# Optimization experiments

Measured on AMD Instinct MI355X. Metric: run time of the kernel, lower is better.

The kernel has to match this reference:

```python
import jax, jax.numpy as jnp
import numpy as np

B, G, D, E = 16, 2048, 2048, 32          # batch, genes, drug fp dim, gene embed dim
NL, NM, H, GS = 16, 4, 6, 64             # n leaves, n mids, term hidden, genes per leaf
GAMMA, NDRUG, EPS = 0.5, 1024, 1e-5

def _bn3(x):  # BatchNorm1d on [B, C, L], training stats, affine at init (gamma=1, beta=0)
    m = x.mean(axis=(0, 2), keepdims=True)
    v = x.var(axis=(0, 2), keepdims=True)
    return (x - m) / jnp.sqrt(v + EPS)

def _bn2(x):  # BatchNorm1d on [B, C]
    m = x.mean(axis=0, keepdims=True)
    v = x.var(axis=0, keepdims=True)
    return (x - m) / jnp.sqrt(v + EPS)

def _term(ci, W1, b1, Wc, bc, Wd, bd):
    # ci: [B, E, in] child input; returns ([B,H,E] 3d out, [B,H] 2d out)
    h = jnp.einsum('bei,hi->bhe', ci, W1) + b1[None, :, None]      # linear -> permute
    h = _bn3(h)
    c = jnp.einsum('bhe,kh->bke', h, Wc) + bc[None, :, None]       # context layer
    out3d = _bn3(c)                                                # [B,H,E]
    mean = out3d.mean(axis=1)                                      # [B,E]
    out2d = _bn2(jnp.tanh(mean @ Wd.T + bd))                       # dimension layer
    return out3d, out2d

def setup_inputs():
    key = jax.random.key(0)
    ks = iter(jax.random.split(key, 64))
    def rn(shape):
        return jax.random.normal(next(ks), shape, dtype=jnp.float32) * 0.05
    x = jax.random.normal(next(ks), (B, G + D + 1), dtype=jnp.float32)
    idx = jax.random.randint(next(ks), (B,), 0, NDRUG)
    x = x.at[:, -1].set(idx.astype(jnp.float32))
    table = jax.random.randint(next(ks), (NDRUG, G), 0, G, dtype=jnp.int32)
    inp = dict(x=x, table=table,
        W_rbf=rn((E, G)), b_rbf=rn((E,)), emb=rn((G, E)),
        W_dg=rn((NL, GS, G)), b_dg=rn((NL, GS)),
        Wl1=rn((NL, H, GS)), bl1=rn((NL, H)), Wlc=rn((NL, H, H)), blc=rn((NL, H)),
        Wld=rn((NL, H, E)), bld=rn((NL, H)),
        Wm1=rn((NM, H, 4 * H)), bm1=rn((NM, H)), Wmc=rn((NM, H, H)), bmc=rn((NM, H)),
        Wmd=rn((NM, H, E)), bmd=rn((NM, H)),
        Wr1=rn((H, 4 * H)), br1=rn((H,)), Wrc=rn((H, H)), brc=rn((H,)),
        Wrd=rn((H, E)), brd=rn((H,)),
        Wd1=rn((100, D)), bd1=rn((100,)), Wd2=rn((50, 100)), bd2=rn((50,)),
        Wd3=rn((H, 50)), bd3=rn((H,)),
        Wf=rn((6, 2 * H)), bf=rn((6,)), Wfa=rn((1, 6)), bfa=rn((1,)),
        Wfo=rn((1, 1)), bfo=rn((1,)))
    return inp

def reference(x, W_rbf, b_rbf, emb, W_dg, b_dg,
              Wl1, bl1, Wlc, blc, Wld, bld,
              Wm1, bm1, Wmc, bmc, Wmd, bmd,
              Wr1, br1, Wrc, brc, Wrd, brd,
              Wd1, bd1, Wd2, bd2, Wd3, bd3,
              Wf, bf, Wfa, bfa, Wfo, bfo, table):
    g = x[:, :G]
    drug = x[:, G:G + D]
    idx = x[:, G + D].astype(jnp.int32)
    # RBF kernel: [B, G, G]
    vect = jnp.exp(-GAMMA * jnp.square(g[:, :, None] - g[:, None, :]))
    gv = jnp.einsum('bij,ej->bie', vect, W_rbf) + b_rbf            # [B,G,E]
    lv = emb[table[idx]]                                            # [B,G,E]
    gf = (gv + lv).transpose(0, 2, 1)                               # [B,E,G]
    # per-leaf direct gene layers
    gene_out = jnp.einsum('beg,lkg->lbek', gf, W_dg) + b_dg[:, None, None, :]  # [NL,B,E,GS]
    leaf3d, _ = jax.vmap(_term)(gene_out, Wl1, bl1, Wlc, blc, Wld, bld)        # [NL,B,H,E]
    # mid terms: concat 4 leaf children along feature dim
    a = leaf3d.transpose(0, 1, 3, 2).reshape(NM, 4, B, E, H)
    a = jnp.moveaxis(a, 1, 3).reshape(NM, B, E, 4 * H)
    mid3d, _ = jax.vmap(_term)(a, Wm1, bm1, Wmc, bmc, Wmd, bmd)                # [NM,B,H,E]
    r = jnp.moveaxis(mid3d.transpose(0, 1, 3, 2), 0, 2).reshape(B, E, 4 * H)
    _, root2d = _term(r, Wr1, br1, Wrc, brc, Wrd, brd)                          # [B,H]
    # drug MLP
    d = drug
    for Wl, bl in ((Wd1, bd1), (Wd2, bd2), (Wd3, bd3)):
        d = _bn2(jnp.tanh(d @ Wl.T + bl))
    fin = jnp.concatenate([root2d, d], axis=1)                                  # [B,2H]
    out = _bn2(jnp.tanh(fin @ Wf.T + bf))
    aux = jnp.tanh(out @ Wfa.T + bfa)
    return aux @ Wfo.T + bfo                                                    # [B,1]
```

## Files before the change

### kernel.cpp

```cpp
#include <hip/hip_runtime.h>
#include <hip/hip_bf16.h>

#define Bb 16
#define Gg 2048
#define Dd 2048
#define XS 4097
#define EPSf 1e-5f
#define CEXP (-0.72134752044448170368f)

typedef unsigned int u32;
typedef __attribute__((ext_vector_type(8))) short bf16x8;
typedef __attribute__((ext_vector_type(4))) float f32x4;

union U16 { uint4 u; bf16x8 v; };

__device__ inline float fast_exp2(float x) {
#if __has_builtin(__builtin_amdgcn_exp2f)
  return __builtin_amdgcn_exp2f(x);
#else
  return exp2f(x);
#endif
}

__device__ inline u32 pk2(float a, float b) {
  return __builtin_amdgcn_perm(__float_as_uint(b), __float_as_uint(a), 0x07060302u);
}
__device__ inline float bftrunc(float a) {
  return __uint_as_float(__float_as_uint(a) & 0xFFFF0000u);
}

__device__ inline void split8(const float* f, U16& hi, U16& lo) {
  u32 h[4], l[4];
  #pragma unroll
  for (int p = 0; p < 4; ++p) {
    float a = f[2 * p], b = f[2 * p + 1];
    h[p] = pk2(a, b);
    l[p] = pk2(a - bftrunc(a), b - bftrunc(b));
  }
  hi.u = make_uint4(h[0], h[1], h[2], h[3]);
  lo.u = make_uint4(l[0], l[1], l[2], l[3]);
}

__device__ inline float wred(float v) {
  #pragma unroll
  for (int o = 32; o > 0; o >>= 1) v += __shfl_xor(v, o, 64);
  return v;
}

__global__ __launch_bounds__(256) void k_split(const float* __restrict__ Wrbf,
                                               const float* __restrict__ Wdg,
                                               u32* __restrict__ Rhi, u32* __restrict__ Rlo,
                                               u32* __restrict__ Dhi, u32* __restrict__ Dlo) {
  int c = blockIdx.x * 256 + threadIdx.x;
  const float* src;
  u32 *dhi, *dlo;
  if (c < 8192) {
    int h = c >> 12, ks = (c >> 6) & 63, l = c & 63;
    src = Wrbf + (h * 16 + (l & 15)) * Gg + ks * 32 + (l >> 4) * 8;
    dhi = Rhi + (size_t)c * 4; dlo = Rlo + (size_t)c * 4;
  } else {
    int cc = c - 8192;
    int nf = cc >> 12, ks = (cc >> 6) & 63, l = cc & 63;
    src = Wdg + (size_t)(nf * 16 + (l & 15)) * Gg + ks * 32 + (l >> 4) * 8;
    dhi = Dhi + (size_t)cc * 4; dlo = Dlo + (size_t)cc * 4;
  }
  float4 f0 = *(const float4*)src;
  float4 f1 = *(const float4*)(src + 4);
  float f[8] = {f0.x, f0.y, f0.z, f0.w, f1.x, f1.y, f1.z, f1.w};
  U16 hi, lo;
  split8(f, hi, lo);
  *(uint4*)dhi = hi.u;
  *(uint4*)dlo = lo.u;
}

__global__ __launch_bounds__(1024) void k_rbf2(const float* __restrict__ x,
                                               const u32* __restrict__ Whi,
                                               const u32* __restrict__ Wlo,
                                               const int* __restrict__ table,
                                               const float* __restrict__ emb,
                                               const float* __restrict__ brbf,
                                               u32* __restrict__ Ahi,
                                               u32* __restrict__ Alo) {
  __shared__ float g_s[2048];
  __shared__ float red[16][64][8];
  const int tid = threadIdx.x;
  const int lane = tid & 63, wid = tid >> 6;
  const int isub = wid >> 2, jcw = wid & 3;
  const int i0 = blockIdx.x * 64, b = blockIdx.y;
  const int i0w = i0 + isub * 16;
  g_s[tid] = x[(size_t)b * XS + tid];
  g_s[tid + 1024] = x[(size_t)b * XS + 1024 + tid];
  const float gi = x[(size_t)b * XS + i0w + (lane & 15)];
  f32x4 acc0 = {0.f, 0.f, 0.f, 0.f};
  f32x4 acc1 = {0.f, 0.f, 0.f, 0.f};
  const int jb = (lane >> 4) * 8;
  __syncthreads();

  #pragma unroll
  for (int ksl = 0; ksl < 16; ++ksl) {
    const int ks = jcw * 16 + ksl;
    const float* gp = &g_s[ks * 32 + jb];
    float4 gja = *(const float4*)gp;
    float4 gjb = *(const float4*)(gp + 4);
    float gv[8] = {gja.x, gja.y, gja.z, gja.w, gjb.x, gjb.y, gjb.z, gjb.w};
    float kv[8];
    #pragma unroll
    for (int q = 0; q < 8; ++q) {
      float d = gi - gv[q];
      kv[q] = fast_exp2(d * d * CEXP);
    }
    U16 ah, al;
    split8(kv, ah, al);
    U16 w0h, w1h, w0l, w1l;
    const size_t wo = (size_t)ks * 256 + lane * 4;
    w0h.u = *(const uint4*)(Whi + wo);
    w1h.u = *(const uint4*)(Whi + 16384 + wo);
    w0l.u = *(const uint4*)(Wlo + wo);
    w1l.u = *(const uint4*)(Wlo + 16384 + wo);
    acc0 = __builtin_amdgcn_mfma_f32_16x16x32_bf16(ah.v, w0h.v, acc0, 0, 0, 0);
    acc0 = __builtin_amdgcn_mfma_f32_16x16x32_bf16(al.v, w0h.v, acc0, 0, 0, 0);
    acc0 = __builtin_amdgcn_mfma_f32_16x16x32_bf16(ah.v, w0l.v, acc0, 0, 0, 0);
    acc1 = __builtin_amdgcn_mfma_f32_16x16x32_bf16(ah.v, w1h.v, acc1, 0, 0, 0);
    acc1 = __builtin_amdgcn_mfma_f32_16x16x32_bf16(al.v, w1h.v, acc1, 0, 0, 0);
    acc1 = __builtin_amdgcn_mfma_f32_16x16x32_bf16(ah.v, w1l.v, acc1, 0, 0, 0);
  }
  #pragma unroll
  for (int k = 0; k < 4; ++k) { red[wid][lane][k] = acc0[k]; red[wid][lane][4 + k] = acc1[k]; }
  __syncthreads();
  if (jcw == 0) {
    float f[8];
    #pragma unroll
    for (int k = 0; k < 8; ++k)
      f[k] = red[isub * 4][lane][k] + red[isub * 4 + 1][lane][k] +
             red[isub * 4 + 2][lane][k] + red[isub * 4 + 3][lane][k];
    const int idx = (int)x[(size_t)b * XS + Gg + Dd];
    const int eloc = lane & 15, quad = lane >> 4;
    const int ib = i0w + quad * 4;
    int4 tt = *(const int4*)&table[(size_t)idx * Gg + ib];
    const int ks = i0w >> 5;
    const int lp = (2 * ((i0w >> 4) & 1) + (quad >> 1)) * 16 + eloc;
    const int hs = quad & 1;
    #pragma unroll
    for (int hb = 0; hb < 2; ++hb) {
      const int e = hb * 16 + eloc;
      const float bias = brbf[e];
      float v0 = f[hb * 4 + 0] + bias + emb[tt.x * 32 + e];
      float v1 = f[hb * 4 + 1] + bias + emb[tt.y * 32 + e];
      float v2 = f[hb * 4 + 2] + bias + emb[tt.z * 32 + e];
      float v3 = f[hb * 4 + 3] + bias + emb[tt.w * 32 + e];
      size_t off = (((size_t)(b * 2 + hb) * 64 + ks) * 64 + lp) * 4 + hs * 2;
      Ahi[off]     = pk2(v0, v1);
      Ahi[off + 1] = pk2(v2, v3);
      Alo[off]     = pk2(v0 - bftrunc(v0), v1 - bftrunc(v1));
      Alo[off + 1] = pk2(v2 - bftrunc(v2), v3 - bftrunc(v3));
    }
  }
}

__global__ __launch_bounds__(512) void k_mm(const u32* __restrict__ Ahi,
                                            const u32* __restrict__ Alo,
                                            const u32* __restrict__ Bhi,
                                            const u32* __restrict__ Blo,
                                            float* __restrict__ part) {
  __shared__ u32 s_mm[6144];
  const int tid = threadIdx.x;
  const int lane = tid & 63, wid = tid >> 6;
  const int id = blockIdx.x;
  const int pl = id & 7, by = (id >> 3) & 7, ph = id >> 6;
  const int p = ph * 8 + pl;
  const int bx = p >> 2, kc = p & 3;
  const int wm = wid >> 2, wn = wid & 3;
  f32x4 acc[2][2];
  #pragma unroll
  for (int mf = 0; mf < 2; ++mf)
    #pragma unroll
    for (int nf = 0; nf < 2; ++nf) acc[mf][nf] = (f32x4){0.f, 0.f, 0.f, 0.f};

  uint4 pf[3];
  #pragma unroll
  for (int q = 0; q < 3; ++q) {
    int seg = wid * 3 + q;
    const u32* src;
    if (seg < 8) {
      int hl = seg >> 2, mf = seg & 3;
      src = (hl ? Alo : Ahi) + (((size_t)(by * 4 + mf) * 64 + kc * 16) * 64 + lane) * 4;
    } else {
      int t = seg - 8, hl = t >> 3, nf = t & 7;
      src = (hl ? Blo : Bhi) + (((size_t)(bx * 8 + nf) * 64 + kc * 16) * 64 + lane) * 4;
    }
    pf[q] = *(const uint4*)src;
  }
  for (int stage = 0; stage < 16; ++stage) {
    __syncthreads();
    #pragma unroll
    for (int q = 0; q < 3; ++q)
      *(uint4*)&s_mm[(wid * 3 + q) * 256 + lane * 4] = pf[q];
    if (stage < 15) {
      const int ks = kc * 16 + stage + 1;
      #pragma unroll
      for (int q = 0; q < 3; ++q) {
        int seg = wid * 3 + q;
        const u32* src;
        if (seg < 8) {
          int hl = seg >> 2, mf = seg & 3;
          src = (hl ? Alo : Ahi) + (((size_t)(by * 4 + mf) * 64 + ks) * 64 + lane) * 4;
        } else {
          int t = seg - 8, hl = t >> 3, nf = t & 7;
          src = (hl ? Blo : Bhi) + (((size_t)(bx * 8 + nf) * 64 + ks) * 64 + lane) * 4;
        }
        pf[q] = *(const uint4*)src;
      }
    }
    __syncthreads();
    U16 ah[2], al[2], bh[2], bl[2];
    #pragma unroll
    for (int mf = 0; mf < 2; ++mf) {
      ah[mf].u = *(const uint4*)&s_mm[(0 + wm * 2 + mf) * 256 + lane * 4];
      al[mf].u = *(const uint4*)&s_mm[(4 + wm * 2 + mf) * 256 + lane * 4];
    }
    #pragma unroll
    for (int nf = 0; nf < 2; ++nf) {
      bh[nf].u = *(const uint4*)&s_mm[(8 + wn * 2 + nf) * 256 + lane * 4];
      bl[nf].u = *(const uint4*)&s_mm[(16 + wn * 2 + nf) * 256 + lane * 4];
    }
    #pragma unroll
    for (int mf = 0; mf < 2; ++mf) {
      #pragma unroll
      for (int nf = 0; nf < 2; ++nf) {
        acc[mf][nf] = __builtin_amdgcn_mfma_f32_16x16x32_bf16(ah[mf].v, bh[nf].v, acc[mf][nf], 0, 0, 0);
        acc[mf][nf] = __builtin_amdgcn_mfma_f32_16x16x32_bf16(al[mf].v, bh[nf].v, acc[mf][nf], 0, 0, 0);
        acc[mf][nf] = __builtin_amdgcn_mfma_f32_16x16x32_bf16(ah[mf].v, bl[nf].v, acc[mf][nf], 0, 0, 0);
      }
    }
  }
  const int quad = lane >> 4, nl = lane & 15;
  #pragma unroll
  for (int mf = 0; mf < 2; ++mf) {
    #pragma unroll
    for (int nf = 0; nf < 2; ++nf) {
      int n  = bx * 128 + wn * 32 + nf * 16 + nl;
      int m0 = by * 64 + wm * 32 + mf * 16 + quad * 4;
      float4 st = make_float4(acc[mf][nf][0], acc[mf][nf][1], acc[mf][nf][2], acc[mf][nf][3]);
      *(float4*)&part[(size_t)kc * 524288 + (size_t)n * 512 + m0] = st;
    }
  }
}

__device__ inline void bn512(float* v, int wv, int lane,
                             float (*r1)[6], float (*r2)[6]) {
  float s[6], q[6];
  #pragma unroll
  for (int c = 0; c < 6; ++c) {
    float a = v[c];
    s[c] = wred(a);
    q[c] = wred(a * a);
  }
  __syncthreads();
  if (lane == 0) {
    #pragma unroll
    for (int c = 0; c < 6; ++c) { r1[wv][c] = s[c]; r2[wv][c] = q[c]; }
  }
  __syncthreads();
  #pragma unroll
  for (int c = 0; c < 6; ++c) {
    float S = 0.f, Q = 0.f;
    #pragma unroll
    for (int w = 0; w < 8; ++w) { S += r1[w][c]; Q += r2[w][c]; }
    float m  = S * (1.0f / 512.0f);
    float va = Q * (1.0f / 512.0f) - m * m;
    v[c] = (v[c] - m) * rsqrtf(va + EPSf);
  }
}

__global__ __launch_bounds__(512) void k_leaf(const float* __restrict__ part,
                                              const float* __restrict__ bdg,
                                              const float* __restrict__ W1,
                                              const float* __restrict__ b1,
                                              const float* __restrict__ Wc,
                                              const float* __restrict__ bc,
                                              float* __restrict__ outp) {
  const int l = blockIdx.x, tid = threadIdx.x;
  const int wv = tid >> 6, lane = tid & 63;
  __shared__ float r1[8][6], r2[8][6];
  float cv[64];
  #pragma unroll
  for (int i = 0; i < 64; ++i) {
    int n = l * 64 + i;
    const float* pp = part + (size_t)n * 512 + tid;
    cv[i] = pp[0] + pp[524288] + pp[2 * 524288] + pp[3 * 524288] + bdg[n];
  }
  const float* w1 = W1 + l * 6 * 64;
  float h[6];
  #pragma unroll
  for (int hh = 0; hh < 6; ++hh) {
    float s = b1[l * 6 + hh];
    #pragma unroll
    for (int i = 0; i < 64; ++i) s = fmaf(cv[i], w1[hh * 64 + i], s);
    h[hh] = s;
  }
  bn512(h, wv, lane, r1, r2);
  float c[6];
  #pragma unroll
  for (int k = 0; k < 6; ++k) {
    float s = bc[l * 6 + k];
    #pragma unroll
    for (int hh = 0; hh < 6; ++hh) s = fmaf(h[hh], Wc[l * 36 + k * 6 + hh], s);
    c[k] = s;
  }
  bn512(c, wv, lane, r1, r2);
  float* o = outp + (((size_t)(l >> 2) * 512 + tid) * 24 + (l & 3) * 6);
  #pragma unroll
  for (int k = 0; k < 6; ++k) o[k] = c[k];
}

__global__ __launch_bounds__(512) void k_mid(const float* __restrict__ gin,
                                             const float* __restrict__ W1,
                                             const float* __restrict__ b1,
                                             const float* __restrict__ Wc,
                                             const float* __restrict__ bc,
                                             float* __restrict__ outp) {
  const int l = blockIdx.x, tid = threadIdx.x;
  const int wv = tid >> 6, lane = tid & 63;
  __shared__ float r1[8][6], r2[8][6];
  const float* ci = gin + ((size_t)l * 512 + tid) * 24;
  float cv[24];
  #pragma unroll
  for (int q = 0; q < 6; ++q) *(float4*)&cv[q * 4] = ((const float4*)ci)[q];
  const float* w1 = W1 + l * 6 * 24;
  float h[6];
  #pragma unroll
  for (int hh = 0; hh < 6; ++hh) {
    float s = b1[l * 6 + hh];
    #pragma unroll
    for (int i = 0; i < 24; ++i) s = fmaf(cv[i], w1[hh * 24 + i], s);
    h[hh] = s;
  }
  bn512(h, wv, lane, r1, r2);
  float c[6];
  #pragma unroll
  for (int k = 0; k < 6; ++k) {
    float s = bc[l * 6 + k];
    #pragma unroll
    for (int hh = 0; hh < 6; ++hh) s = fmaf(h[hh], Wc[l * 36 + k * 6 + hh], s);
    c[k] = s;
  }
  bn512(c, wv, lane, r1, r2);
  float* o = outp + ((size_t)tid * 24 + l * 6);
  #pragma unroll
  for (int k = 0; k < 6; ++k) o[k] = c[k];
}

__global__ __launch_bounds__(1024) void k_drug1(const float* __restrict__ x,
                                                const float* __restrict__ Wd1,
                                                const float* __restrict__ bd1,
                                                float* __restrict__ d1) {
  const int c = blockIdx.x;
  const int tid = threadIdx.x;
  const int b = tid >> 6, lane = tid & 63;
  const float* xb = x + (size_t)b * XS + Gg;
  const float* w = Wd1 + (size_t)c * 2048;
  float s = 0.f;
  #pragma unroll
  for (int q = 0; q < 8; ++q) {
    int k = q * 256 + lane * 4;
    float4 xv = *(const float4*)(xb + k);
    float4 wv = *(const float4*)(w + k);
    s = fmaf(xv.x, wv.x, s);
    s = fmaf(xv.y, wv.y, s);
    s = fmaf(xv.z, wv.z, s);
    s = fmaf(xv.w, wv.w, s);
  }
  s = wred(s);
  __shared__ float y[16];
  if (lane == 0) y[b] = tanhf(s + bd1[c]);
  __syncthreads();
  if (tid < 16) {
    float S = 0.f, Q = 0.f;
    #pragma unroll
    for (int bb = 0; bb < 16; ++bb) { float v = y[bb]; S += v; Q += v * v; }
    float m = S * (1.0f / 16.0f), va = Q * (1.0f / 16.0f) - m * m;
    d1[tid * 100 + c] = (y[tid] - m) * rsqrtf(va + EPSf);
  }
}

__global__ __launch_bounds__(512) void k_rootfinal(const float* __restrict__ rootin,
                                                   const float* __restrict__ d1,
                                                   const float* __restrict__ Wr1,
                                                   const float* __restrict__ br1,
                                                   const float* __restrict__ Wrc,
                                                   const float* __restrict__ brc,
                                                   const float* __restrict__ Wrd,
                                                   const float* __restrict__ brd,
                                                   const float* __restrict__ Wd2,
                                                   const float* __restrict__ bd2,
                                                   const float* __restrict__ Wd3,
                                                   const float* __restrict__ bd3,
                                                   const float* __restrict__ Wf,
                                                   const float* __restrict__ bf,
                                                   const float* __restrict__ Wfa,
                                                   const float* __restrict__ bfa,
                                                   const float* __restrict__ Wfo,
                                                   const float* __restrict__ bfo,
                                                   float* __restrict__ out) {
  const int tid = threadIdx.x;
  const int wv = tid >> 6, lane = tid & 63;
  __shared__ float r1[8][6], r2[8][6];
  __shared__ float w2s[50 * 101];
  __shared__ float d1s[1600];
  __shared__ float r2ds[96];
  for (int u = tid; u < 5000; u += 512) w2s[(u / 100) * 101 + (u % 100)] = Wd2[u];
  for (int u = tid; u < 1600; u += 512) d1s[u] = d1[u];

  const float* ci = rootin + (size_t)tid * 24;
  float cv[24];
  #pragma unroll
  for (int q = 0; q < 6; ++q) *(float4*)&cv[q * 4] = ((const float4*)ci)[q];
  float h[6];
  #pragma unroll
  for (int hh = 0; hh < 6; ++hh) {
    float s = br1[hh];
    #pragma unroll
    for (int i = 0; i < 24; ++i) s = fmaf(cv[i], Wr1[hh * 24 + i], s);
    h[hh] = s;
  }
  bn512(h, wv, lane, r1, r2);
  float c[6];
  #pragma unroll
  for (int k = 0; k < 6; ++k) {
    float s = brc[k];
    #pragma unroll
    for (int hh = 0; hh < 6; ++hh) s = fmaf(h[hh], Wrc[k * 6 + hh], s);
    c[k] = s;
  }
  bn512(c, wv, lane, r1, r2);
  float mv = (c[0] + c[1] + c[2] + c[3] + c[4] + c[5]) * (1.0f / 6.0f);
  __shared__ float shm[512];
  shm[tid] = mv;
  __syncthreads();
  __shared__ float st[96];
  if (tid < 96) {
    int b = tid / 6, hh = tid % 6;
    float s = brd[hh];
    #pragma unroll
    for (int e = 0; e < 32; ++e) s = fmaf(shm[b * 32 + e], Wrd[hh * 32 + e], s);
    st[tid] = tanhf(s);
  }
  __syncthreads();
  if (tid < 6) {
    float S = 0.f, Q = 0.f;
    for (int b = 0; b < 16; ++b) { float v = st[b * 6 + tid]; S += v; Q += v * v; }
    float m = S * (1.0f / 16.0f), va = Q * (1.0f / 16.0f) - m * m;
    float iv = rsqrtf(va + EPSf);
    for (int b = 0; b < 16; ++b) r2ds[b * 6 + tid] = (st[b * 6 + tid] - m) * iv;
  }
  __syncthreads();

  __shared__ float s2[800], mu2[50], iv2[50];
  for (int u = tid; u < 800; u += 512) {
    int b = u / 50, cc = u % 50;
    float s = bd2[cc];
    #pragma unroll
    for (int k = 0; k < 100; ++k) s = fmaf(d1s[b * 100 + k], w2s[cc * 101 + k], s);
    s2[u] = tanhf(s);
  }
  __syncthreads();
  if (tid < 50) {
    float S = 0.f, Q = 0.f;
    #pragma unroll
    for (int b = 0; b < 16; ++b) { float v = s2[b * 50 + tid]; S += v; Q += v * v; }
    float m = S * (1.0f / 16.0f), va = Q * (1.0f / 16.0f) - m * m;
    mu2[tid] = m; iv2[tid] = rsqrtf(va + EPSf);
  }
  __syncthreads();
  __shared__ float s3[96], mu3[6], iv3[6];
  if (tid < 96) {
    int b = tid / 6, cc = tid % 6;
    float s = bd3[cc];
    #pragma unroll
    for (int k = 0; k < 50; ++k)
      s = fmaf((s2[b * 50 + k] - mu2[k]) * iv2[k], Wd3[cc * 50 + k], s);
    s3[tid] = tanhf(s);
  }
  __syncthreads();
  if (tid < 6) {
    float S = 0.f, Q = 0.f;
    #pragma unroll
    for (int b = 0; b < 16; ++b) { float v = s3[b * 6 + tid]; S += v; Q += v * v; }
    float m = S * (1.0f / 16.0f), va = Q * (1.0f / 16.0f) - m * m;
    mu3[tid] = m; iv3[tid] = rsqrtf(va + EPSf);
  }
  __syncthreads();
  __shared__ float sf[96], muf[6], ivf[6];
  if (tid < 96) {
    int b = tid / 6, cc = tid % 6;
    float s = bf[cc];
    #pragma unroll
    for (int q = 0; q < 6; ++q) s = fmaf(r2ds[b * 6 + q], Wf[cc * 12 + q], s);
    #pragma unroll
    for (int q = 0; q < 6; ++q)
      s = fmaf((s3[b * 6 + q] - mu3[q]) * iv3[q], Wf[cc * 12 + 6 + q], s);
    sf[tid] = tanhf(s);
  }
  __syncthreads();
  if (tid < 6) {
    float S = 0.f, Q = 0.f;
    #pragma unroll
    for (int b = 0; b < 16; ++b) { float v = sf[b * 6 + tid]; S += v; Q += v * v; }
    float m = S * (1.0f / 16.0f), va = Q * (1.0f / 16.0f) - m * m;
    muf[tid] = m; ivf[tid] = rsqrtf(va + EPSf);
  }
  __syncthreads();
  if (tid < 16) {
    float s = bfa[0];
    #pragma unroll
    for (int q = 0; q < 6; ++q)
      s = fmaf((sf[tid * 6 + q] - muf[q]) * ivf[q], Wfa[q], s);
    float a = tanhf(s);
    out[tid] = a * Wfo[0] + bfo[0];
  }
}

extern "C" void kernel_launch(void* const* d_in, const int* in_sizes, int n_in,
                              void* d_out, int out_size, void* d_ws, size_t ws_size,
                              hipStream_t stream) {
  const float* x     = (const float*)d_in[0];
  const int*   table = (const int*)d_in[1];
  const float* Wrbf  = (const float*)d_in[2];
  const float* brbf  = (const float*)d_in[3];
  const float* emb   = (const float*)d_in[4];
  const float* Wdg   = (const float*)d_in[5];
  const float* bdg   = (const float*)d_in[6];
  const float* Wl1   = (const float*)d_in[7];
  const float* bl1   = (const float*)d_in[8];
  const float* Wlc   = (const float*)d_in[9];
  const float* blc   = (const float*)d_in[10];
  const float* Wm1   = (const float*)d_in[13];
  const float* bm1   = (const float*)d_in[14];
  const float* Wmc   = (const float*)d_in[15];
  const float* bmc   = (const float*)d_in[16];
  const float* Wr1   = (const float*)d_in[19];
  const float* br1   = (const float*)d_in[20];
  const float* Wrc   = (const float*)d_in[21];
  const float* brc   = (const float*)d_in[22];
  const float* Wrd   = (const float*)d_in[23];
  const float* brd   = (const float*)d_in[24];
  const float* Wd1   = (const float*)d_in[25];
  const float* bd1   = (const float*)d_in[26];
  const float* Wd2   = (const float*)d_in[27];
  const float* bd2   = (const float*)d_in[28];
  const float* Wd3   = (const float*)d_in[29];
  const float* bd3   = (const float*)d_in[30];
  const float* Wf    = (const float*)d_in[31];
  const float* bf    = (const float*)d_in[32];
  const float* Wfa   = (const float*)d_in[33];
  const float* bfa   = (const float*)d_in[34];
  const float* Wfo   = (const float*)d_in[35];
  const float* bfo   = (const float*)d_in[36];
  float* out = (float*)d_out;

  u32* Rhi = (u32*)d_ws;
  u32* Rlo = Rhi + 32768;
  u32* Dhi = Rlo + 32768;
  u32* Dlo = Dhi + 1048576;
  u32* Ahi = Dlo + 1048576;
  u32* Alo = Ahi + 524288;
  float* partB = (float*)(Alo + 524288);
  float* midin = partB + 4 * 524288;
  float* rootin= midin + 49152;
  float* d1    = rootin + 12288;

  hipLaunchKernelGGL(k_drug1,     dim3(100),    dim3(1024), 0, stream, x, Wd1, bd1, d1);
  hipLaunchKernelGGL(k_split,     dim3(1056),   dim3(256),  0, stream, Wrbf, Wdg, Rhi, Rlo, Dhi, Dlo);
  hipLaunchKernelGGL(k_rbf2,      dim3(32, 16), dim3(1024), 0, stream, x, Rhi, Rlo, table, emb, brbf, Ahi, Alo);
  hipLaunchKernelGGL(k_mm,        dim3(256),    dim3(512),  0, stream, Ahi, Alo, Dhi, Dlo, partB);
  hipLaunchKernelGGL(k_leaf,      dim3(16),     dim3(512),  0, stream, partB, bdg, Wl1, bl1, Wlc, blc, midin);
  hipLaunchKernelGGL(k_mid,       dim3(4),      dim3(512),  0, stream, midin, Wm1, bm1, Wmc, bmc, rootin);
  hipLaunchKernelGGL(k_rootfinal, dim3(1),      dim3(512),  0, stream, rootin, d1,
                     Wr1, br1, Wrc, brc, Wrd, brd, Wd2, bd2, Wd3, bd3,
                     Wf, bf, Wfa, bfa, Wfo, bfo, out);
}
```

Measured before the change: 115.6 us.

## Merge drug and split kernels, stage rbf weights in LDS, split leaf reduction

```diff
diff --git a/kernel.cpp b/kernel.cpp
--- a/kernel.cpp
+++ b/kernel.cpp
@@ -47,33 +47,67 @@
   return v;
 }
 
-__global__ __launch_bounds__(256) void k_split(const float* __restrict__ Wrbf,
-                                               const float* __restrict__ Wdg,
-                                               u32* __restrict__ Rhi, u32* __restrict__ Rlo,
-                                               u32* __restrict__ Dhi, u32* __restrict__ Dlo) {
-  int c = blockIdx.x * 256 + threadIdx.x;
-  const float* src;
-  u32 *dhi, *dlo;
-  if (c < 8192) {
-    int h = c >> 12, ks = (c >> 6) & 63, l = c & 63;
-    src = Wrbf + (h * 16 + (l & 15)) * Gg + ks * 32 + (l >> 4) * 8;
-    dhi = Rhi + (size_t)c * 4; dlo = Rlo + (size_t)c * 4;
+__global__ __launch_bounds__(1024) void k_pre(const float* __restrict__ x,
+                                              const float* __restrict__ Wd1,
+                                              const float* __restrict__ bd1,
+                                              float* __restrict__ d1,
+                                              const float* __restrict__ Wrbf,
+                                              const float* __restrict__ Wdg,
+                                              u32* __restrict__ Rhi, u32* __restrict__ Rlo,
+                                              u32* __restrict__ Dhi, u32* __restrict__ Dlo) {
+  const int tid = threadIdx.x;
+  if (blockIdx.x < 100) {
+    const int c = blockIdx.x;
+    const int b = tid >> 6, lane = tid & 63;
+    const float* xb = x + (size_t)b * XS + Gg;
+    const float* w = Wd1 + (size_t)c * 2048;
+    float s = 0.f;
+    #pragma unroll
+    for (int q = 0; q < 8; ++q) {
+      int k = q * 256 + lane * 4;
+      float4 xv = *(const float4*)(xb + k);
+      float4 wv = *(const float4*)(w + k);
+      s = fmaf(xv.x, wv.x, s);
+      s = fmaf(xv.y, wv.y, s);
+      s = fmaf(xv.z, wv.z, s);
+      s = fmaf(xv.w, wv.w, s);
+    }
+    s = wred(s);
+    __shared__ float y[16];
+    if (lane == 0) y[b] = tanhf(s + bd1[c]);
+    __syncthreads();
+    if (tid < 16) {
+      float S = 0.f, Q = 0.f;
+      #pragma unroll
+      for (int bb = 0; bb < 16; ++bb) { float v = y[bb]; S += v; Q += v * v; }
+      float m = S * (1.0f / 16.0f), va = Q * (1.0f / 16.0f) - m * m;
+      d1[tid * 100 + c] = (y[tid] - m) * rsqrtf(va + EPSf);
+    }
   } else {
-    int cc = c - 8192;
-    int nf = cc >> 12, ks = (cc >> 6) & 63, l = cc & 63;
-    src = Wdg + (size_t)(nf * 16 + (l & 15)) * Gg + ks * 32 + (l >> 4) * 8;
-    dhi = Dhi + (size_t)cc * 4; dlo = Dlo + (size_t)cc * 4;
-  }
-  float4 f0 = *(const float4*)src;
-  float4 f1 = *(const float4*)(src + 4);
-  float f[8] = {f0.x, f0.y, f0.z, f0.w, f1.x, f1.y, f1.z, f1.w};
-  U16 hi, lo;
-  split8(f, hi, lo);
-  *(uint4*)dhi = hi.u;
-  *(uint4*)dlo = lo.u;
-}
-
-__global__ __launch_bounds__(1024) void k_rbf2(const float* __restrict__ x,
+    int c = (blockIdx.x - 100) * 1024 + tid;
+    const float* src;
+    u32 *dhi, *dlo;
+    if (c < 8192) {
+      int h = c >> 12, ks = (c >> 6) & 63, l = c & 63;
+      src = Wrbf + (h * 16 + (l & 15)) * Gg + ks * 32 + (l >> 4) * 8;
+      dhi = Rhi + (size_t)c * 4; dlo = Rlo + (size_t)c * 4;
+    } else {
+      int cc = c - 8192;
+      int nf = cc >> 12, ks = (cc >> 6) & 63, l = cc & 63;
+      src = Wdg + (size_t)(nf * 16 + (l & 15)) * Gg + ks * 32 + (l >> 4) * 8;
+      dhi = Dhi + (size_t)cc * 4; dlo = Dlo + (size_t)cc * 4;
+    }
+    float4 f0 = *(const float4*)src;
+    float4 f1 = *(const float4*)(src + 4);
+    float f[8] = {f0.x, f0.y, f0.z, f0.w, f1.x, f1.y, f1.z, f1.w};
+    U16 hi, lo;
+    split8(f, hi, lo);
+    *(uint4*)dhi = hi.u;
+    *(uint4*)dlo = lo.u;
+  }
+}
+
+__global__ __launch_bounds__(1024) void k_rbf3(const float* __restrict__ x,
                                                const u32* __restrict__ Whi,
                                                const u32* __restrict__ Wlo,
                                                const int* __restrict__ table,
@@ -82,7 +116,8 @@
                                                u32* __restrict__ Ahi,
                                                u32* __restrict__ Alo) {
   __shared__ float g_s[2048];
-  __shared__ float red[16][64][8];
+  __shared__ u32 w_s[2][16][256];
+  float (*red)[64][8] = (float (*)[64][8]) & w_s[0][0][0];
   const int tid = threadIdx.x;
   const int lane = tid & 63, wid = tid >> 6;
   const int isub = wid >> 2, jcw = wid & 3;
@@ -94,10 +129,16 @@
   f32x4 acc0 = {0.f, 0.f, 0.f, 0.f};
   f32x4 acc1 = {0.f, 0.f, 0.f, 0.f};
   const int jb = (lane >> 4) * 8;
-  __syncthreads();
-
-  #pragma unroll
+
+  const int jcw_s = wid >> 2, arr2_s = wid & 3;
+  const u32* wsrc = ((arr2_s & 2) ? Wlo : Whi) + ((arr2_s & 1) ? 16384 : 0);
+  uint4 pf = *(const uint4*)(wsrc + ((size_t)(jcw_s * 16)) * 256 + lane * 4);
+
   for (int ksl = 0; ksl < 16; ++ksl) {
+    *(uint4*)&w_s[ksl & 1][wid][lane * 4] = pf;
+    if (ksl < 15)
+      pf = *(const uint4*)(wsrc + ((size_t)(jcw_s * 16 + ksl + 1)) * 256 + lane * 4);
+    __syncthreads();
     const int ks = jcw * 16 + ksl;
     const float* gp = &g_s[ks * 32 + jb];
     float4 gja = *(const float4*)gp;
@@ -112,11 +153,10 @@
     U16 ah, al;
     split8(kv, ah, al);
     U16 w0h, w1h, w0l, w1l;
-    const size_t wo = (size_t)ks * 256 + lane * 4;
-    w0h.u = *(const uint4*)(Whi + wo);
-    w1h.u = *(const uint4*)(Whi + 16384 + wo);
-    w0l.u = *(const uint4*)(Wlo + wo);
-    w1l.u = *(const uint4*)(Wlo + 16384 + wo);
+    w0h.u = *(const uint4*)&w_s[ksl & 1][jcw * 4 + 0][lane * 4];
+    w1h.u = *(const uint4*)&w_s[ksl & 1][jcw * 4 + 1][lane * 4];
+    w0l.u = *(const uint4*)&w_s[ksl & 1][jcw * 4 + 2][lane * 4];
+    w1l.u = *(const uint4*)&w_s[ksl & 1][jcw * 4 + 3][lane * 4];
     acc0 = __builtin_amdgcn_mfma_f32_16x16x32_bf16(ah.v, w0h.v, acc0, 0, 0, 0);
     acc0 = __builtin_amdgcn_mfma_f32_16x16x32_bf16(al.v, w0h.v, acc0, 0, 0, 0);
     acc0 = __builtin_amdgcn_mfma_f32_16x16x32_bf16(ah.v, w0l.v, acc0, 0, 0, 0);
@@ -124,6 +164,7 @@
     acc1 = __builtin_amdgcn_mfma_f32_16x16x32_bf16(al.v, w1h.v, acc1, 0, 0, 0);
     acc1 = __builtin_amdgcn_mfma_f32_16x16x32_bf16(ah.v, w1l.v, acc1, 0, 0, 0);
   }
+  __syncthreads();
   #pragma unroll
   for (int k = 0; k < 4; ++k) { red[wid][lane][k] = acc0[k]; red[wid][lane][4 + k] = acc1[k]; }
   __syncthreads();
@@ -272,31 +313,43 @@
   }
 }
 
-__global__ __launch_bounds__(512) void k_leaf(const float* __restrict__ part,
-                                              const float* __restrict__ bdg,
-                                              const float* __restrict__ W1,
-                                              const float* __restrict__ b1,
-                                              const float* __restrict__ Wc,
-                                              const float* __restrict__ bc,
-                                              float* __restrict__ outp) {
+__global__ __launch_bounds__(512) void k_leafA(const float* __restrict__ part,
+                                               const float* __restrict__ bdg,
+                                               const float* __restrict__ W1,
+                                               float* __restrict__ hpart) {
+  const int ic = blockIdx.x, l = blockIdx.y, tid = threadIdx.x;
+  const float* w1 = W1 + l * 384;
+  float hp[6] = {0.f, 0.f, 0.f, 0.f, 0.f, 0.f};
+  #pragma unroll
+  for (int r = 0; r < 8; ++r) {
+    int i = ic * 8 + r;
+    int n = l * 64 + i;
+    const float* pp = part + (size_t)n * 512 + tid;
+    float cv = pp[0] + pp[524288] + pp[2 * 524288] + pp[3 * 524288] + bdg[n];
+    #pragma unroll
+    for (int hh = 0; hh < 6; ++hh) hp[hh] = fmaf(cv, w1[hh * 64 + i], hp[hh]);
+  }
+  float* o = hpart + ((size_t)(l * 8 + ic) * 512 + tid) * 6;
+  #pragma unroll
+  for (int hh = 0; hh < 6; ++hh) o[hh] = hp[hh];
+}
+
+__global__ __launch_bounds__(512) void k_leafB(const float* __restrict__ hpart,
+                                               const float* __restrict__ b1,
+                                               const float* __restrict__ Wc,
+                                               const float* __restrict__ bc,
+                                               float* __restrict__ outp) {
   const int l = blockIdx.x, tid = threadIdx.x;
   const int wv = tid >> 6, lane = tid & 63;
   __shared__ float r1[8][6], r2[8][6];
-  float cv[64];
-  #pragma unroll
-  for (int i = 0; i < 64; ++i) {
-    int n = l * 64 + i;
-    const float* pp = part + (size_t)n * 512 + tid;
-    cv[i] = pp[0] + pp[524288] + pp[2 * 524288] + pp[3 * 524288] + bdg[n];
-  }
-  const float* w1 = W1 + l * 6 * 64;
   float h[6];
   #pragma unroll
-  for (int hh = 0; hh < 6; ++hh) {
-    float s = b1[l * 6 + hh];
-    #pragma unroll
-    for (int i = 0; i < 64; ++i) s = fmaf(cv[i], w1[hh * 64 + i], s);
-    h[hh] = s;
+  for (int hh = 0; hh < 6; ++hh) h[hh] = b1[l * 6 + hh];
+  #pragma unroll
+  for (int ic = 0; ic < 8; ++ic) {
+    const float* hp = hpart + ((size_t)(l * 8 + ic) * 512 + tid) * 6;
+    #pragma unroll
+    for (int hh = 0; hh < 6; ++hh) h[hh] += hp[hh];
   }
   bn512(h, wv, lane, r1, r2);
   float c[6];
@@ -348,39 +401,6 @@
   float* o = outp + ((size_t)tid * 24 + l * 6);
   #pragma unroll
   for (int k = 0; k < 6; ++k) o[k] = c[k];
-}
-
-__global__ __launch_bounds__(1024) void k_drug1(const float* __restrict__ x,
-                                                const float* __restrict__ Wd1,
-                                                const float* __restrict__ bd1,
-                                                float* __restrict__ d1) {
-  const int c = blockIdx.x;
-  const int tid = threadIdx.x;
-  const int b = tid >> 6, lane = tid & 63;
-  const float* xb = x + (size_t)b * XS + Gg;
-  const float* w = Wd1 + (size_t)c * 2048;
-  float s = 0.f;
-  #pragma unroll
-  for (int q = 0; q < 8; ++q) {
-    int k = q * 256 + lane * 4;
-    float4 xv = *(const float4*)(xb + k);
-    float4 wv = *(const float4*)(w + k);
-    s = fmaf(xv.x, wv.x, s);
-    s = fmaf(xv.y, wv.y, s);
-    s = fmaf(xv.z, wv.z, s);
-    s = fmaf(xv.w, wv.w, s);
-  }
-  s = wred(s);
-  __shared__ float y[16];
-  if (lane == 0) y[b] = tanhf(s + bd1[c]);
-  __syncthreads();
-  if (tid < 16) {
-    float S = 0.f, Q = 0.f;
-    #pragma unroll
-    for (int bb = 0; bb < 16; ++bb) { float v = y[bb]; S += v; Q += v * v; }
-    float m = S * (1.0f / 16.0f), va = Q * (1.0f / 16.0f) - m * m;
-    d1[tid * 100 + c] = (y[tid] - m) * rsqrtf(va + EPSf);
-  }
 }
 
 __global__ __launch_bounds__(512) void k_rootfinal(const float* __restrict__ rootin,
@@ -565,15 +585,18 @@
   u32* Ahi = Dlo + 1048576;
   u32* Alo = Ahi + 524288;
   float* partB = (float*)(Alo + 524288);
-  float* midin = partB + 4 * 524288;
+  float* hpart = partB + 4 * 524288;
+  float* midin = hpart + 393216;
   float* rootin= midin + 49152;
   float* d1    = rootin + 12288;
 
-  hipLaunchKernelGGL(k_drug1,     dim3(100),    dim3(1024), 0, stream, x, Wd1, bd1, d1);
-  hipLaunchKernelGGL(k_split,     dim3(1056),   dim3(256),  0, stream, Wrbf, Wdg, Rhi, Rlo, Dhi, Dlo);
-  hipLaunchKernelGGL(k_rbf2,      dim3(32, 16), dim3(1024), 0, stream, x, Rhi, Rlo, table, emb, brbf, Ahi, Alo);
+  hipLaunchKernelGGL(k_pre,       dim3(364),    dim3(1024), 0, stream,
+                     x, Wd1, bd1, d1, Wrbf, Wdg, Rhi, Rlo, Dhi, Dlo);
+  hipLaunchKernelGGL(k_rbf3,      dim3(32, 16), dim3(1024), 0, stream,
+                     x, Rhi, Rlo, table, emb, brbf, Ahi, Alo);
   hipLaunchKernelGGL(k_mm,        dim3(256),    dim3(512),  0, stream, Ahi, Alo, Dhi, Dlo, partB);
-  hipLaunchKernelGGL(k_leaf,      dim3(16),     dim3(512),  0, stream, partB, bdg, Wl1, bl1, Wlc, blc, midin);
+  hipLaunchKernelGGL(k_leafA,     dim3(8, 16),  dim3(512),  0, stream, partB, bdg, Wl1, hpart);
+  hipLaunchKernelGGL(k_leafB,     dim3(16),     dim3(512),  0, stream, hpart, bl1, Wlc, blc, midin);
   hipLaunchKernelGGL(k_mid,       dim3(4),      dim3(512),  0, stream, midin, Wm1, bm1, Wmc, bmc, rootin);
   hipLaunchKernelGGL(k_rootfinal, dim3(1),      dim3(512),  0, stream, rootin, d1,
                      Wr1, br1, Wrc, brc, Wrd, brd, Wd2, bd2, Wd3, bd3,
```

Result: faster. 104.7 us, median of 2 (-9.4%).
